# Kernel tuning notes

Measured on AMD Instinct MI355X. Metric: run time of the kernel, lower is better.

The kernel has to match this reference:

```python
import jax, jax.numpy as jnp
import numpy as np

UNITS = 20
EPS_GPE_STN = 0.1


def _w_lateral(units=UNITS, eps=EPS_GPE_STN):
    # Faithful port of generate_distance_matrix: grid_size = int(sqrt(units))
    grid_size = int(units ** 0.5)
    idx = np.arange(units)
    xi, yi = np.divmod(idx, grid_size)
    d = (xi[:, None] - xi[None, :]) ** 2 + (yi[:, None] - yi[None, :]) ** 2
    return jnp.asarray(np.exp(-d.astype(np.float32) / eps), dtype=jnp.float32)


def setup_inputs() -> dict:
    key = jax.random.key(0)
    ks = jax.random.split(key, 8)
    B = 524288
    k = 1.0 / np.sqrt(UNITS)  # PyTorch LSTMCell init scale
    x = jax.random.normal(ks[0], (B, UNITS), dtype=jnp.float32)
    h = jax.random.normal(ks[1], (B, UNITS), dtype=jnp.float32)
    c = jax.random.normal(ks[2], (B, UNITS), dtype=jnp.float32)
    W_ih = jax.random.uniform(ks[3], (4 * UNITS, UNITS), jnp.float32, -k, k)
    W_hh = jax.random.uniform(ks[4], (4 * UNITS, UNITS), jnp.float32, -k, k)
    b_ih = jax.random.uniform(ks[5], (4 * UNITS,), jnp.float32, -k, k)
    b_hh = jax.random.uniform(ks[6], (4 * UNITS,), jnp.float32, -k, k)
    W_lat = _w_lateral()
    return {"x": x, "h": h, "c": c, "W_ih": W_ih, "W_hh": W_hh,
            "b_ih": b_ih, "b_hh": b_hh, "W_lat": W_lat}


def reference(x, h, c, W_ih, W_hh, b_ih, b_hh, W_lat):
    # nn.LSTMCell: gates in (i, f, g, o) order
    gates = x @ W_ih.T + h @ W_hh.T + (b_ih + b_hh)  # [B, 4U]
    i, f, g, o = jnp.split(gates, 4, axis=-1)
    c_next = jax.nn.sigmoid(f) * c + jax.nn.sigmoid(i) * jnp.tanh(g)
    h_lstm = jax.nn.sigmoid(o) * jnp.tanh(c_next)
    # bmm(W_lateral, h[:, :, None]).squeeze(-1) == h @ W_lat.T, then tanh
    h_next = jnp.tanh(h_lstm @ W_lat.T)
    return (h_next, c_next)
```

## Files before the change

kernel.cpp:

```cpp
#include <hip/hip_runtime.h>

#define UNITS 20

typedef __attribute__((ext_vector_type(8))) short short8;
typedef __attribute__((ext_vector_type(4))) float floatx4;
typedef unsigned int u32;
typedef unsigned short u16;

__device__ __forceinline__ float rcpf_fast(float x) { return __builtin_amdgcn_rcpf(x); }
__device__ __forceinline__ float sigmoidf_fast(float x) { return rcpf_fast(1.0f + __expf(-x)); }
__device__ __forceinline__ float tanhf_fast(float x) { return 1.0f - 2.0f * rcpf_fast(1.0f + __expf(2.0f * x)); }

__device__ __forceinline__ u32 f2bf(float f) {
  u32 u = __builtin_bit_cast(u32, f);
  u += 0x7fffu + ((u >> 16) & 1u);
  return u >> 16;
}
__device__ __forceinline__ u32 pack2(float a, float b) { return f2bf(a) | (f2bf(b) << 16); }

__global__ void prep_kernel(const float* __restrict__ W_ih, const float* __restrict__ W_hh,
                            const float* __restrict__ b_ih, const float* __restrict__ b_hh,
                            const float* __restrict__ W_lat,
                            u16* __restrict__ fragsG, u16* __restrict__ fragsL,
                            float4* __restrict__ bias4) {
  int tid = threadIdx.x;
  for (int e = tid; e < 768; e += 256) {
    int fi = e >> 6, lane = e & 63;
    int r = lane & 15, q = lane >> 4;
    short8 v8;
    if (fi < 10) {
      int t = fi >> 1, cc = fi & 1;
      int gr = (r & 3) * 20 + (r >> 2) * 5 + t;
#pragma unroll
      for (int j = 0; j < 8; ++j) {
        int k = cc * 32 + q * 8 + j;
        float v = 0.0f;
        if (k < 20) v = W_ih[gr * UNITS + k];
        else if (k < 40) v = W_hh[gr * UNITS + (k - 20)];
        v8[j] = (short)f2bf(v);
      }
      *(short8*)(fragsG + (size_t)e * 8) = v8;
    } else {
      int t = fi - 10;
      int vr = t * 16 + r;
#pragma unroll
      for (int j = 0; j < 8; ++j) {
        int k = q * 8 + j;
        float v = (vr < 20 && k < 20) ? W_lat[vr * UNITS + k] : 0.0f;
        v8[j] = (short)f2bf(v);
      }
      *(short8*)(fragsL + (size_t)(t * 64 + lane) * 8) = v8;
    }
  }
  if (tid < 20)
    bias4[tid] = make_float4(b_ih[tid] + b_hh[tid],
                             b_ih[20 + tid] + b_hh[20 + tid],
                             b_ih[40 + tid] + b_hh[40 + tid],
                             b_ih[60 + tid] + b_hh[60 + tid]);
}

#define SZE 72
#define SHL 40

__global__ __launch_bounds__(256) void stn_main(
    const float* __restrict__ x, const float* __restrict__ h, const float* __restrict__ c,
    const u16* __restrict__ fragsG, const u16* __restrict__ fragsL,
    const float4* __restrict__ bias4, float* __restrict__ out, int B) {
  __shared__ unsigned char smem[19456];
  u16*   Zs = (u16*)smem;
  float* Cn = (float*)smem;
  float* Cs = (float*)(smem + 9216);
  float* Hn = (float*)(smem + 9216);
  u16*   Hl = (u16*)(smem + 14336);

  const int tid  = threadIdx.x;
  const int lane = tid & 63;
  const int wv   = tid >> 6;
  const int m = lane & 15, q = lane >> 4;
  const long rowBase = (long)blockIdx.x * 64;
  const int  myrow = wv * 16 + m;
  const long f4base = rowBase * 5;
  const long f4max = (long)B * 5 - 1;

  {
    const float4* x4 = (const float4*)x;
    const float4* h4 = (const float4*)h;
    const float4* c4 = (const float4*)c;
    for (int e = tid; e < 320; e += 256) {
      long gi = f4base + e; if (gi > f4max) gi = f4max;
      int row = e / 5, part = e - row * 5;
      float4 vx = x4[gi];
      u32* zp = (u32*)(Zs + row * SZE + part * 4);
      zp[0] = pack2(vx.x, vx.y); zp[1] = pack2(vx.z, vx.w);
      float4 vh = h4[gi];
      u32* zq = (u32*)(Zs + row * SZE + 20 + part * 4);
      zq[0] = pack2(vh.x, vh.y); zq[1] = pack2(vh.z, vh.w);
      ((float4*)Cs)[e] = c4[gi];
    }
    int r = tid & 63, s = tid >> 6;
    u32* zp = (u32*)(Zs + r * SZE + 40);
    zp[s * 3 + 0] = 0; zp[s * 3 + 1] = 0; zp[s * 3 + 2] = 0;
    u32* hp = (u32*)(Hl + r * SHL + 20);
    hp[s] = 0; if (s < 2) hp[s + 4] = 0;
  }
  __syncthreads();

  short8 bfr[2];
#pragma unroll
  for (int cc = 0; cc < 2; ++cc)
    bfr[cc] = *(const short8*)(Zs + myrow * SZE + cc * 32 + q * 8);

  floatx4 acc[5];
#pragma unroll
  for (int t = 0; t < 5; ++t) {
    float4 b4 = bias4[q * 5 + t];
    acc[t] = (floatx4){b4.x, b4.y, b4.z, b4.w};
#pragma unroll
    for (int cc = 0; cc < 2; ++cc) {
      short8 af = *(const short8*)(fragsG + (size_t)((t * 2 + cc) * 64 + lane) * 8);
      acc[t] = __builtin_amdgcn_mfma_f32_16x16x32_bf16(af, bfr[cc], acc[t], 0, 0, 0);
    }
  }

  float cnv[5];
#pragma unroll
  for (int t = 0; t < 5; ++t) {
    int u = q * 5 + t;
    float ig = sigmoidf_fast(acc[t][0]);
    float fg = sigmoidf_fast(acc[t][1]);
    float gg = tanhf_fast(acc[t][2]);
    float og = sigmoidf_fast(acc[t][3]);
    float cv = Cs[myrow * 20 + u];
    float cn = fg * cv + ig * gg;
    cnv[t] = cn;
    Hl[myrow * SHL + u] = (u16)f2bf(og * tanhf_fast(cn));
  }
  __syncthreads();

  short8 bl = *(const short8*)(Hl + myrow * SHL + q * 8);
  floatx4 accL[2];
#pragma unroll
  for (int t = 0; t < 2; ++t) {
    short8 al = *(const short8*)(fragsL + (size_t)(t * 64 + lane) * 8);
    accL[t] = __builtin_amdgcn_mfma_f32_16x16x32_bf16(al, bl, (floatx4){0.f, 0.f, 0.f, 0.f}, 0, 0, 0);
  }

#pragma unroll
  for (int t = 0; t < 5; ++t) Cn[myrow * 20 + q * 5 + t] = cnv[t];
#pragma unroll
  for (int t = 0; t < 2; ++t)
#pragma unroll
    for (int reg = 0; reg < 4; ++reg) {
      int v = t * 16 + q * 4 + reg;
      if (v < 20) Hn[myrow * 20 + v] = tanhf_fast(accL[t][reg]);
    }
  __syncthreads();

  {
    float4* outh4 = (float4*)out;
    float4* outc4 = (float4*)(out + (size_t)B * UNITS);
    for (int e = tid; e < 320; e += 256) {
      long gi = f4base + e;
      if (gi <= f4max) {
        outh4[gi] = ((const float4*)Hn)[e];
        outc4[gi] = ((const float4*)Cn)[e];
      }
    }
  }
}

extern "C" void kernel_launch(void* const* d_in, const int* in_sizes, int n_in,
                              void* d_out, int out_size, void* d_ws, size_t ws_size,
                              hipStream_t stream) {
  const float* x     = (const float*)d_in[0];
  const float* h     = (const float*)d_in[1];
  const float* c     = (const float*)d_in[2];
  const float* W_ih  = (const float*)d_in[3];
  const float* W_hh  = (const float*)d_in[4];
  const float* b_ih  = (const float*)d_in[5];
  const float* b_hh  = (const float*)d_in[6];
  const float* W_lat = (const float*)d_in[7];
  float* out = (float*)d_out;

  u16*    fragsG = (u16*)d_ws;
  u16*    fragsL = (u16*)((char*)d_ws + 10240);
  float4* bias4  = (float4*)((char*)d_ws + 12288);

  int B = in_sizes[0] / UNITS;
  prep_kernel<<<1, 256, 0, stream>>>(W_ih, W_hh, b_ih, b_hh, W_lat, fragsG, fragsL, bias4);
  int grid = (B + 63) / 64;
  stn_main<<<grid, 256, 0, stream>>>(x, h, c, fragsG, fragsL, bias4, out, B);
}
```

Measured before the change: 204.4 us.

## Load MFMA operands directly from global memory and drop block-wide LDS staging

Each lane now reads its x/h row slices straight from global memory into MFMA B-fragments and reads c directly into registers. The shared tile staging and all __syncthreads are removed; only a small per-wave LDS buffer for the lateral matmul input remains, ordered with an lgkmcnt wait. Outputs are written directly from registers rather than through LDS. This removes LDS round trips and barriers but gives up the fully coalesced float4 staging: global accesses are now strided per lane and c stores are scalar.

```diff
diff --git a/kernel.cpp b/kernel.cpp
--- a/kernel.cpp
+++ b/kernel.cpp
@@ -4,6 +4,7 @@
 
 typedef __attribute__((ext_vector_type(8))) short short8;
 typedef __attribute__((ext_vector_type(4))) float floatx4;
+typedef __attribute__((ext_vector_type(4))) unsigned int u32x4;
 typedef unsigned int u32;
 typedef unsigned short u16;
 
@@ -17,6 +18,12 @@
   return u >> 16;
 }
 __device__ __forceinline__ u32 pack2(float a, float b) { return f2bf(a) | (f2bf(b) << 16); }
+__device__ __forceinline__ short8 pack8(float4 a, float4 b) {
+  u32x4 w;
+  w[0] = pack2(a.x, a.y); w[1] = pack2(a.z, a.w);
+  w[2] = pack2(b.x, b.y); w[3] = pack2(b.z, b.w);
+  return __builtin_bit_cast(short8, w);
+}
 
 __global__ void prep_kernel(const float* __restrict__ W_ih, const float* __restrict__ W_hh,
                             const float* __restrict__ b_ih, const float* __restrict__ b_hh,
@@ -59,113 +66,83 @@
                              b_ih[60 + tid] + b_hh[60 + tid]);
 }
 
-#define SZE 72
-#define SHL 40
-
 __global__ __launch_bounds__(256) void stn_main(
     const float* __restrict__ x, const float* __restrict__ h, const float* __restrict__ c,
     const u16* __restrict__ fragsG, const u16* __restrict__ fragsL,
     const float4* __restrict__ bias4, float* __restrict__ out, int B) {
-  __shared__ unsigned char smem[19456];
-  u16*   Zs = (u16*)smem;
-  float* Cn = (float*)smem;
-  float* Cs = (float*)(smem + 9216);
-  float* Hn = (float*)(smem + 9216);
-  u16*   Hl = (u16*)(smem + 14336);
+  __shared__ u16 HlAll[4][16 * 40];
 
-  const int tid  = threadIdx.x;
+  const int tid = threadIdx.x;
   const int lane = tid & 63;
-  const int wv   = tid >> 6;
+  const int wv = tid >> 6;
   const int m = lane & 15, q = lane >> 4;
-  const long rowBase = (long)blockIdx.x * 64;
-  const int  myrow = wv * 16 + m;
-  const long f4base = rowBase * 5;
-  const long f4max = (long)B * 5 - 1;
+  u16* Hl = HlAll[wv];
 
-  {
-    const float4* x4 = (const float4*)x;
-    const float4* h4 = (const float4*)h;
-    const float4* c4 = (const float4*)c;
-    for (int e = tid; e < 320; e += 256) {
-      long gi = f4base + e; if (gi > f4max) gi = f4max;
-      int row = e / 5, part = e - row * 5;
-      float4 vx = x4[gi];
-      u32* zp = (u32*)(Zs + row * SZE + part * 4);
-      zp[0] = pack2(vx.x, vx.y); zp[1] = pack2(vx.z, vx.w);
-      float4 vh = h4[gi];
-      u32* zq = (u32*)(Zs + row * SZE + 20 + part * 4);
-      zq[0] = pack2(vh.x, vh.y); zq[1] = pack2(vh.z, vh.w);
-      ((float4*)Cs)[e] = c4[gi];
-    }
-    int r = tid & 63, s = tid >> 6;
-    u32* zp = (u32*)(Zs + r * SZE + 40);
-    zp[s * 3 + 0] = 0; zp[s * 3 + 1] = 0; zp[s * 3 + 2] = 0;
-    u32* hp = (u32*)(Hl + r * SHL + 20);
-    hp[s] = 0; if (s < 2) hp[s + 4] = 0;
-  }
-  __syncthreads();
+  const long row = (long)blockIdx.x * 64 + wv * 16 + m;
+  const bool live = row < B;
+  const long rowc = live ? row : (long)(B - 1);
 
-  short8 bfr[2];
+  const float4* x4 = (const float4*)x + rowc * 5;
+  const float4* h4 = (const float4*)h + rowc * 5;
+  int j0 = q * 2;
+  float4 f0 = (j0 < 5) ? x4[j0] : h4[j0 - 5];
+  float4 f1 = (j0 + 1 < 5) ? x4[j0 + 1] : h4[j0 - 4];
+  short8 bfr0 = pack8(f0, f1);
+  short8 bfr1 = (short8){0, 0, 0, 0, 0, 0, 0, 0};
+  if (q == 0) bfr1 = pack8(h4[3], h4[4]);
+
+  const float* cp = c + rowc * 20 + q * 5;
+  float cvv[5];
 #pragma unroll
-  for (int cc = 0; cc < 2; ++cc)
-    bfr[cc] = *(const short8*)(Zs + myrow * SZE + cc * 32 + q * 8);
+  for (int t = 0; t < 5; ++t) cvv[t] = cp[t];
 
   floatx4 acc[5];
 #pragma unroll
   for (int t = 0; t < 5; ++t) {
     float4 b4 = bias4[q * 5 + t];
     acc[t] = (floatx4){b4.x, b4.y, b4.z, b4.w};
-#pragma unroll
-    for (int cc = 0; cc < 2; ++cc) {
-      short8 af = *(const short8*)(fragsG + (size_t)((t * 2 + cc) * 64 + lane) * 8);
-      acc[t] = __builtin_amdgcn_mfma_f32_16x16x32_bf16(af, bfr[cc], acc[t], 0, 0, 0);
-    }
+    short8 af0 = *(const short8*)(fragsG + (size_t)((t * 2 + 0) * 64 + lane) * 8);
+    acc[t] = __builtin_amdgcn_mfma_f32_16x16x32_bf16(af0, bfr0, acc[t], 0, 0, 0);
+    short8 af1 = *(const short8*)(fragsG + (size_t)((t * 2 + 1) * 64 + lane) * 8);
+    acc[t] = __builtin_amdgcn_mfma_f32_16x16x32_bf16(af1, bfr1, acc[t], 0, 0, 0);
+  }
+
+  {
+    u16* zp = Hl + m * 40 + 20 + q * 3;
+    zp[0] = 0; zp[1] = 0; zp[2] = 0;
   }
 
   float cnv[5];
 #pragma unroll
   for (int t = 0; t < 5; ++t) {
-    int u = q * 5 + t;
     float ig = sigmoidf_fast(acc[t][0]);
     float fg = sigmoidf_fast(acc[t][1]);
     float gg = tanhf_fast(acc[t][2]);
     float og = sigmoidf_fast(acc[t][3]);
-    float cv = Cs[myrow * 20 + u];
-    float cn = fg * cv + ig * gg;
+    float cn = fg * cvv[t] + ig * gg;
     cnv[t] = cn;
-    Hl[myrow * SHL + u] = (u16)f2bf(og * tanhf_fast(cn));
-  }
-  __syncthreads();
-
-  short8 bl = *(const short8*)(Hl + myrow * SHL + q * 8);
-  floatx4 accL[2];
-#pragma unroll
-  for (int t = 0; t < 2; ++t) {
-    short8 al = *(const short8*)(fragsL + (size_t)(t * 64 + lane) * 8);
-    accL[t] = __builtin_amdgcn_mfma_f32_16x16x32_bf16(al, bl, (floatx4){0.f, 0.f, 0.f, 0.f}, 0, 0, 0);
+    Hl[m * 40 + q * 5 + t] = (u16)f2bf(og * tanhf_fast(cn));
   }
 
+  asm volatile("s_waitcnt lgkmcnt(0)" ::: "memory");
+
+  short8 bl = *(const short8*)(Hl + m * 40 + q * 8);
+  short8 al0 = *(const short8*)(fragsL + (size_t)(0 * 64 + lane) * 8);
+  short8 al1 = *(const short8*)(fragsL + (size_t)(1 * 64 + lane) * 8);
+  floatx4 z4 = (floatx4){0.f, 0.f, 0.f, 0.f};
+  floatx4 accL0 = __builtin_amdgcn_mfma_f32_16x16x32_bf16(al0, bl, z4, 0, 0, 0);
+  floatx4 accL1 = __builtin_amdgcn_mfma_f32_16x16x32_bf16(al1, bl, z4, 0, 0, 0);
+
+  if (live) {
+    float* oh = out + row * 20;
+    float* oc = out + (size_t)B * 20 + row * 20;
+    *(float4*)(oh + q * 4) = make_float4(tanhf_fast(accL0[0]), tanhf_fast(accL0[1]),
+                                         tanhf_fast(accL0[2]), tanhf_fast(accL0[3]));
+    if (q == 0)
+      *(float4*)(oh + 16) = make_float4(tanhf_fast(accL1[0]), tanhf_fast(accL1[1]),
+                                        tanhf_fast(accL1[2]), tanhf_fast(accL1[3]));
 #pragma unroll
-  for (int t = 0; t < 5; ++t) Cn[myrow * 20 + q * 5 + t] = cnv[t];
-#pragma unroll
-  for (int t = 0; t < 2; ++t)
-#pragma unroll
-    for (int reg = 0; reg < 4; ++reg) {
-      int v = t * 16 + q * 4 + reg;
-      if (v < 20) Hn[myrow * 20 + v] = tanhf_fast(accL[t][reg]);
-    }
-  __syncthreads();
-
-  {
-    float4* outh4 = (float4*)out;
-    float4* outc4 = (float4*)(out + (size_t)B * UNITS);
-    for (int e = tid; e < 320; e += 256) {
-      long gi = f4base + e;
-      if (gi <= f4max) {
-        outh4[gi] = ((const float4*)Hn)[e];
-        outc4[gi] = ((const float4*)Cn)[e];
-      }
-    }
+    for (int t = 0; t < 5; ++t) oc[q * 5 + t] = cnv[t];
   }
 }
 
```

Measured after the change: 208.5 us. +2.0%, slower.
